# Kernel tuning notes

Measured on AMD Instinct MI355X. Metric: run time of the kernel, lower is better.

Reference implementation:

```python
import jax, jax.numpy as jnp
import numpy as np

N_NODES = 100000
N_EDGES = 1600000
D = 128


def setup_inputs() -> dict:
    key = jax.random.key(0)
    ks = jax.random.split(key, 8)
    s = lambda fan_in: 1.0 / np.sqrt(fan_in)
    return {
        "node_feature": jax.random.normal(ks[0], (N_NODES, D), dtype=jnp.float32),
        "src": jax.random.randint(ks[1], (N_EDGES,), 0, N_NODES),
        "dst": jax.random.randint(ks[2], (N_EDGES,), 0, N_NODES),
        "W1": jax.random.normal(ks[3], (2 * D, D), dtype=jnp.float32) * s(2 * D),
        "b1": jnp.zeros((D,), dtype=jnp.float32),
        "W2": jax.random.normal(ks[4], (D, D), dtype=jnp.float32) * s(D),
        "b2": jnp.zeros((D,), dtype=jnp.float32),
        "W3": jax.random.normal(ks[5], (D, D), dtype=jnp.float32) * s(D),
        "b3": jnp.zeros((D,), dtype=jnp.float32),
    }


def reference(node_feature, src, dst, W1, b1, W2, b2, W3, b3):
    n_nodes = node_feature.shape[0]
    # message: gather src node features over edges  [E, D]
    msg = node_feature[src]
    # reduce: sum messages into destination nodes   [N, D]
    agg = jax.ops.segment_sum(msg, dst, num_segments=n_nodes)
    # apply: concat(aggregated, own) -> MLP         [N, 2D] -> [N, D]
    inp = jnp.concatenate([agg, node_feature], axis=-1)
    h = jax.nn.relu(inp @ W1 + b1)
    h = jax.nn.relu(h @ W2 + b2)
    return h @ W3 + b3
```

## Files before the change

### kernel.cpp

```cpp
#include <hip/hip_runtime.h>

#define NNODES 100000
#define NEDGES 1600000
#define DD 128
#define BM 64
#define NBUCK 98
#define NBLK_MLP ((NNODES + BM - 1) / BM)
#define CAP 32
#define CAPB 20480
#define BIN1_WGS 391
#define BIN1_EPW 4096

#define WS_GCUR 100000
#define WS_BBASE 100128
#define WS_OFFS 100352
#define WS_ESRC 201216

#define WT1HI 0
#define WT1LO 32768
#define WT2HI 65536
#define WT2LO 81920
#define WT3HI 98304
#define WT3LO 114688

typedef __attribute__((ext_vector_type(8))) short short8;
typedef __attribute__((ext_vector_type(4))) float f32x4;

__device__ __forceinline__ void bf16_split(float x, ushort& hi, ushort& lo) {
  unsigned u = __float_as_uint(x);
  ushort h = (ushort)((u + 0x7FFFu + ((u >> 16) & 1u)) >> 16);
  float r = x - __uint_as_float(((unsigned)h) << 16);
  unsigned v = __float_as_uint(r);
  ushort l = (ushort)((v + 0x7FFFu + ((v >> 16) & 1u)) >> 16);
  hi = h;
  lo = l;
}

__device__ __forceinline__ void split8(const float4 v0, const float4 v1,
                                       short8& hi, short8& lo) {
  float x[8] = {v0.x, v0.y, v0.z, v0.w, v1.x, v1.y, v1.z, v1.w};
#pragma unroll
  for (int j = 0; j < 8; ++j) {
    ushort h, l;
    bf16_split(x[j], h, l);
    hi[j] = (short)h;
    lo[j] = (short)l;
  }
}

__global__ __launch_bounds__(256) void bin1_kernel(const int* __restrict__ src,
                                                   const int* __restrict__ dst,
                                                   int* __restrict__ gcur,
                                                   unsigned* __restrict__ ebuf) {
  __shared__ unsigned stage[NBUCK][CAP];
  __shared__ int scnt[NBUCK];
  const int t = threadIdx.x;
  for (int i = t; i < NBUCK; i += 256) scnt[i] = 0;
  __syncthreads();
  const int e0 = blockIdx.x * BIN1_EPW;
  for (int r = 0; r < BIN1_EPW / 1024; ++r) {
    unsigned item[4];
    int buck[4];
    int pend[4];
#pragma unroll
    for (int j = 0; j < 4; ++j) {
      pend[j] = 0;
      int e = e0 + r * 1024 + j * 256 + t;
      if (e < NEDGES) {
        int d = dst[e];
        int s = src[e];
        buck[j] = d >> 10;
        item[j] = ((unsigned)(d & 1023) << 17) | (unsigned)s;
        int p = atomicAdd(&scnt[buck[j]], 1);
        if (p < CAP)
          stage[buck[j]][p] = item[j];
        else
          pend[j] = 1;
      }
    }
    int pendLeft;
    do {
      __syncthreads();
      if (t < NBUCK && scnt[t] >= CAP) {
        int base = t * CAPB + atomicAdd(&gcur[t], CAP);
        for (int q = 0; q < CAP; ++q) ebuf[base + q] = stage[t][q];
        scnt[t] = 0;
      }
      __syncthreads();
      int mypend = 0;
#pragma unroll
      for (int j = 0; j < 4; ++j) {
        if (pend[j]) {
          int p = atomicAdd(&scnt[buck[j]], 1);
          if (p < CAP) {
            stage[buck[j]][p] = item[j];
            pend[j] = 0;
          } else {
            mypend = 1;
          }
        }
      }
      pendLeft = __syncthreads_count(mypend);
    } while (pendLeft > 0);
  }
  __syncthreads();
  if (t < NBUCK) {
    int n = scnt[t];
    if (n > 0) {
      int base = t * CAPB + atomicAdd(&gcur[t], n);
      for (int q = 0; q < n; ++q) ebuf[base + q] = stage[t][q];
    }
  }
}

__global__ __launch_bounds__(128) void bscan_kernel(const int* __restrict__ gcur,
                                                    int* __restrict__ bbase,
                                                    int* __restrict__ offs) {
  __shared__ int s[128];
  const int t = threadIdx.x;
  int v = (t < NBUCK) ? gcur[t] : 0;
  s[t] = v;
  __syncthreads();
  for (int off = 1; off < 128; off <<= 1) {
    int u = (t >= off) ? s[t - off] : 0;
    __syncthreads();
    s[t] += u;
    __syncthreads();
  }
  if (t < NBUCK) bbase[t] = s[t] - v;
  if (t == NBUCK - 1) offs[NNODES] = s[t];
}

__global__ __launch_bounds__(1024) void bucket_csr_kernel(const unsigned* __restrict__ ebuf,
                                                          const int* __restrict__ gcur,
                                                          const int* __restrict__ bbase,
                                                          int* __restrict__ offs,
                                                          int* __restrict__ esrc) {
  __shared__ int h[1024];
  __shared__ int cur[1024];
  const int t = threadIdx.x;
  const int c = blockIdx.x;
  const int n = gcur[c];
  const unsigned* eb = ebuf + c * CAPB;
  h[t] = 0;
  __syncthreads();
  for (int i = t; i < n; i += 1024) atomicAdd(&h[eb[i] >> 17], 1);
  __syncthreads();
  int v = h[t];
  for (int off = 1; off < 1024; off <<= 1) {
    int u = (t >= off) ? h[t - off] : 0;
    __syncthreads();
    h[t] += u;
    __syncthreads();
  }
  int excl = h[t] - v + bbase[c];
  int node = (c << 10) + t;
  if (node < NNODES) offs[node] = excl;
  cur[t] = excl;
  __syncthreads();
  for (int i = t; i < n; i += 1024) {
    unsigned e = eb[i];
    int p = atomicAdd(&cur[e >> 17], 1);
    esrc[p] = (int)(e & 0x1FFFFu);
  }
}

__global__ __launch_bounds__(256) void wprep_kernel(const float* __restrict__ W1,
                                                    const float* __restrict__ W2,
                                                    const float* __restrict__ W3,
                                                    ushort* __restrict__ wt) {
  int tid = blockIdx.x * 256 + threadIdx.x;
  const float* W;
  int dstHi, dstLo, k, col;
  if (tid < 32768) {
    int j = tid & 7, l = (tid >> 3) & 63, tile = tid >> 9;
    int kk = tile & 7, c16 = tile >> 3;
    k = kk * 32 + (l >> 4) * 8 + j;
    col = c16 * 16 + (l & 15);
    W = W1;
    dstHi = WT1HI + tid;
    dstLo = WT1LO + tid;
  } else {
    int t2 = tid - 32768;
    int which = t2 >> 14;
    int t1 = t2 & 16383;
    int j = t1 & 7, l = (t1 >> 3) & 63, tile = t1 >> 9;
    int kk = tile & 3, c16 = tile >> 2;
    k = kk * 32 + (l >> 4) * 8 + j;
    col = c16 * 16 + (l & 15);
    W = which ? W3 : W2;
    dstHi = (which ? WT3HI : WT2HI) + t1;
    dstLo = (which ? WT3LO : WT2LO) + t1;
  }
  ushort hi, lo;
  bf16_split(W[k * DD + col], hi, lo);
  wt[dstHi] = hi;
  wt[dstLo] = lo;
}


template <int KT>
__device__ __forceinline__ void lds_ksteps(const ushort* Hh, const ushort* Hl,
                                           const ushort* __restrict__ WhiT,
                                           const ushort* __restrict__ WloT,
                                           int tileOff, int wc2, int lane,
                                           int l15, int lhi, f32x4 acc[4][2]) {
#pragma unroll 2
  for (int kk = 0; kk < 4; ++kk) {
    short8 bhi[2], blo[2];
#pragma unroll
    for (int ct = 0; ct < 2; ++ct) {
      int tb = ((wc2 + ct) * KT + tileOff + kk) * 512 + lane * 8;
      bhi[ct] = *(const short8*)&WhiT[tb];
      blo[ct] = *(const short8*)&WloT[tb];
    }
#pragma unroll
    for (int rt = 0; rt < 4; ++rt) {
      int row = rt * 16 + l15;
      int byte = (row * 256 + kk * 64 + lhi * 16) ^ ((row & 7) << 4);
      short8 ahi = *(const short8*)((const char*)Hh + byte);
      short8 alo = *(const short8*)((const char*)Hl + byte);
#pragma unroll
      for (int ct = 0; ct < 2; ++ct) {
        acc[rt][ct] = __builtin_amdgcn_mfma_f32_16x16x32_bf16(ahi, bhi[ct], acc[rt][ct], 0, 0, 0);
        acc[rt][ct] = __builtin_amdgcn_mfma_f32_16x16x32_bf16(ahi, blo[ct], acc[rt][ct], 0, 0, 0);
        acc[rt][ct] = __builtin_amdgcn_mfma_f32_16x16x32_bf16(alo, bhi[ct], acc[rt][ct], 0, 0, 0);
      }
    }
  }
}

__device__ __forceinline__ void l1_step(const float* __restrict__ srcb,
                                        const ushort* __restrict__ wt,
                                        int kkTile, int kOff, const int rowA[4],
                                        int wc2, int lane, int lhi,
                                        f32x4 acc[4][2]) {
  short8 bhi[2], blo[2];
#pragma unroll
  for (int ct = 0; ct < 2; ++ct) {
    int tb = ((wc2 + ct) * 8 + kkTile) * 512 + lane * 8;
    bhi[ct] = *(const short8*)&wt[WT1HI + tb];
    blo[ct] = *(const short8*)&wt[WT1LO + tb];
  }
#pragma unroll
  for (int rt = 0; rt < 4; ++rt) {
    const float* p = srcb + rowA[rt] * DD + kOff + lhi * 8;
    float4 v0 = *(const float4*)p;
    float4 v1 = *(const float4*)(p + 4);
    short8 ahi, alo;
    split8(v0, v1, ahi, alo);
#pragma unroll
    for (int ct = 0; ct < 2; ++ct) {
      acc[rt][ct] = __builtin_amdgcn_mfma_f32_16x16x32_bf16(ahi, bhi[ct], acc[rt][ct], 0, 0, 0);
      acc[rt][ct] = __builtin_amdgcn_mfma_f32_16x16x32_bf16(ahi, blo[ct], acc[rt][ct], 0, 0, 0);
      acc[rt][ct] = __builtin_amdgcn_mfma_f32_16x16x32_bf16(alo, bhi[ct], acc[rt][ct], 0, 0, 0);
    }
  }
}

__device__ __forceinline__ void store_h(ushort* Hh, ushort* Hl,
                                        const float* __restrict__ b,
                                        int wc2, int l15, int lhi,
                                        f32x4 acc[4][2]) {
#pragma unroll
  for (int rt = 0; rt < 4; ++rt) {
#pragma unroll
    for (int ct = 0; ct < 2; ++ct) {
      int col = (wc2 + ct) * 16 + l15;
      float bias = b[col];
#pragma unroll
      for (int i = 0; i < 4; ++i) {
        int row = rt * 16 + lhi * 4 + i;
        float v = fmaxf(acc[rt][ct][i] + bias, 0.f);
        ushort h, l;
        bf16_split(v, h, l);
        int byte = (row * 256 + col * 2) ^ ((row & 7) << 4);
        *(ushort*)((char*)Hh + byte) = h;
        *(ushort*)((char*)Hl + byte) = l;
      }
    }
  }
}

__global__ __launch_bounds__(256, 5) void fused_kernel(const float* __restrict__ nf,
                                                       const int* __restrict__ offs,
                                                       const int* __restrict__ esrc,
                                                       const ushort* __restrict__ wt,
                                                       const float* __restrict__ b1,
                                                       const float* __restrict__ b2,
                                                       const float* __restrict__ b3,
                                                       float* __restrict__ out) {
  __shared__ ushort smem[16384];
  ushort* Xhi = smem;
  ushort* Xlo = smem + 8192;

  const int t = threadIdx.x;
  const int lane = t & 63;
  const int w = t >> 6;
  const int wc2 = w * 2;
  const int l15 = lane & 15;
  const int lhi = lane >> 4;
  const int base = blockIdx.x * BM;

  {
    const int g = t >> 5;
    const int l32 = t & 31;
    const int col = l32 << 2;
    for (int j = 0; j < 8; ++j) {
      const int r = g * 8 + j;
      const int node = base + r;
      if (node >= NNODES) break;
      float4 a0 = make_float4(0.f, 0.f, 0.f, 0.f);
      float4 a1 = make_float4(0.f, 0.f, 0.f, 0.f);
      float4 a2 = make_float4(0.f, 0.f, 0.f, 0.f);
      float4 a3 = make_float4(0.f, 0.f, 0.f, 0.f);
      const int beg = offs[node];
      const int end = offs[node + 1];
      int i = beg;
      int s0, s1, s2, s3;
      const bool have4 = (i + 3 < end);
      if (have4) {
        s0 = esrc[i]; s1 = esrc[i + 1]; s2 = esrc[i + 2]; s3 = esrc[i + 3];
      }
      for (; i + 7 < end; i += 4) {
        int n0 = esrc[i + 4], n1 = esrc[i + 5], n2 = esrc[i + 6], n3 = esrc[i + 7];
        float4 v0 = *(const float4*)&nf[s0 * DD + col];
        float4 v1 = *(const float4*)&nf[s1 * DD + col];
        float4 v2 = *(const float4*)&nf[s2 * DD + col];
        float4 v3 = *(const float4*)&nf[s3 * DD + col];
        a0.x += v0.x; a0.y += v0.y; a0.z += v0.z; a0.w += v0.w;
        a1.x += v1.x; a1.y += v1.y; a1.z += v1.z; a1.w += v1.w;
        a2.x += v2.x; a2.y += v2.y; a2.z += v2.z; a2.w += v2.w;
        a3.x += v3.x; a3.y += v3.y; a3.z += v3.z; a3.w += v3.w;
        s0 = n0; s1 = n1; s2 = n2; s3 = n3;
      }
      if (have4) {
        float4 v0 = *(const float4*)&nf[s0 * DD + col];
        float4 v1 = *(const float4*)&nf[s1 * DD + col];
        float4 v2 = *(const float4*)&nf[s2 * DD + col];
        float4 v3 = *(const float4*)&nf[s3 * DD + col];
        a0.x += v0.x; a0.y += v0.y; a0.z += v0.z; a0.w += v0.w;
        a1.x += v1.x; a1.y += v1.y; a1.z += v1.z; a1.w += v1.w;
        a2.x += v2.x; a2.y += v2.y; a2.z += v2.z; a2.w += v2.w;
        a3.x += v3.x; a3.y += v3.y; a3.z += v3.z; a3.w += v3.w;
        i += 4;
      }
      for (; i < end; ++i) {
        int s = esrc[i];
        float4 v0 = *(const float4*)&nf[s * DD + col];
        a0.x += v0.x; a0.y += v0.y; a0.z += v0.z; a0.w += v0.w;
      }
      a0.x += a1.x; a0.y += a1.y; a0.z += a1.z; a0.w += a1.w;
      a2.x += a3.x; a2.y += a3.y; a2.z += a3.z; a2.w += a3.w;
      a0.x += a2.x; a0.y += a2.y; a0.z += a2.z; a0.w += a2.w;
      ushort h0, h1, h2, h3, l0, l1, l2, l3;
      bf16_split(a0.x, h0, l0);
      bf16_split(a0.y, h1, l1);
      bf16_split(a0.z, h2, l2);
      bf16_split(a0.w, h3, l3);
      int byte = (r * 256 + col * 2) ^ ((r & 7) << 4);
      *(ushort4*)((char*)Xhi + byte) = make_ushort4(h0, h1, h2, h3);
      *(ushort4*)((char*)Xlo + byte) = make_ushort4(l0, l1, l2, l3);
    }
  }
  __syncthreads();

  int rowA[4];
#pragma unroll
  for (int rt = 0; rt < 4; ++rt) rowA[rt] = min(base + rt * 16 + l15, NNODES - 1);

  const f32x4 z = {0.f, 0.f, 0.f, 0.f};
  f32x4 acc[4][2];

#pragma unroll
  for (int rt = 0; rt < 4; ++rt)
#pragma unroll
    for (int ct = 0; ct < 2; ++ct) acc[rt][ct] = z;
  lds_ksteps<8>(Xhi, Xlo, wt + WT1HI, wt + WT1LO, 0, wc2, lane, l15, lhi, acc);
#pragma unroll 2
  for (int kk = 0; kk < 4; ++kk)
    l1_step(nf, wt, kk + 4, kk * 32, rowA, wc2, lane, lhi, acc);
  __syncthreads();
  store_h(Xhi, Xlo, b1, wc2, l15, lhi, acc);
  __syncthreads();

#pragma unroll
  for (int rt = 0; rt < 4; ++rt)
#pragma unroll
    for (int ct = 0; ct < 2; ++ct) acc[rt][ct] = z;
  lds_ksteps<4>(Xhi, Xlo, wt + WT2HI, wt + WT2LO, 0, wc2, lane, l15, lhi, acc);
  __syncthreads();
  store_h(Xhi, Xlo, b2, wc2, l15, lhi, acc);
  __syncthreads();

#pragma unroll
  for (int rt = 0; rt < 4; ++rt)
#pragma unroll
    for (int ct = 0; ct < 2; ++ct) acc[rt][ct] = z;
  lds_ksteps<4>(Xhi, Xlo, wt + WT3HI, wt + WT3LO, 0, wc2, lane, l15, lhi, acc);
#pragma unroll
  for (int rt = 0; rt < 4; ++rt) {
#pragma unroll
    for (int ct = 0; ct < 2; ++ct) {
      int col = (wc2 + ct) * 16 + l15;
      float bias = b3[col];
#pragma unroll
      for (int i = 0; i < 4; ++i) {
        int row = base + rt * 16 + lhi * 4 + i;
        if (row < NNODES) out[row * DD + col] = acc[rt][ct][i] + bias;
      }
    }
  }
}

extern "C" void kernel_launch(void* const* d_in, const int* in_sizes, int n_in,
                              void* d_out, int out_size, void* d_ws, size_t ws_size,
                              hipStream_t stream) {
  const float* nf = (const float*)d_in[0];
  const int* src = (const int*)d_in[1];
  const int* dst = (const int*)d_in[2];
  const float* W1 = (const float*)d_in[3];
  const float* b1 = (const float*)d_in[4];
  const float* W2 = (const float*)d_in[5];
  const float* b2 = (const float*)d_in[6];
  const float* W3 = (const float*)d_in[7];
  const float* b3 = (const float*)d_in[8];
  float* out = (float*)d_out;

  int* wsi = (int*)d_ws;
  int* gcur = wsi + WS_GCUR;
  int* bbase = wsi + WS_BBASE;
  int* offs = wsi + WS_OFFS;
  int* esrc = wsi + WS_ESRC;
  ushort* wt = (ushort*)wsi;

  unsigned* ebuf = (unsigned*)out;

  hipMemsetAsync(gcur, 0, NBUCK * sizeof(int), stream);
  bin1_kernel<<<BIN1_WGS, 256, 0, stream>>>(src, dst, gcur, ebuf);
  bscan_kernel<<<1, 128, 0, stream>>>(gcur, bbase, offs);
  bucket_csr_kernel<<<NBUCK, 1024, 0, stream>>>(ebuf, gcur, bbase, offs, esrc);
  wprep_kernel<<<256, 256, 0, stream>>>(W1, W2, W3, wt);
  fused_kernel<<<NBLK_MLP, 256, 0, stream>>>(nf, offs, esrc, wt, b1, b2, b3, out);
}
```

Baseline: 240.0 us.

## Double fused block to 512 threads with dynamic row assignment for aggregation

The fused gather+MLP kernel now runs 8 waves per block instead of 4. Each wave computes one 16-column strip instead of two, which halves per-thread accumulators. During aggregation, half-wave groups claim rows dynamically through an LDS atomic counter, so rows with many edges are load-balanced across groups. This costs an extra barrier and per-row atomics, and each wave now re-reads the same A fragments from LDS and global memory for fewer columns.

Measured after the change: 257.7 us. 7.4% more time.

```diff
diff --git a/kernel.cpp b/kernel.cpp
--- a/kernel.cpp
+++ b/kernel.cpp
@@ -199,90 +199,7 @@
 }
 
 
-template <int KT>
-__device__ __forceinline__ void lds_ksteps(const ushort* Hh, const ushort* Hl,
-                                           const ushort* __restrict__ WhiT,
-                                           const ushort* __restrict__ WloT,
-                                           int tileOff, int wc2, int lane,
-                                           int l15, int lhi, f32x4 acc[4][2]) {
-#pragma unroll 2
-  for (int kk = 0; kk < 4; ++kk) {
-    short8 bhi[2], blo[2];
-#pragma unroll
-    for (int ct = 0; ct < 2; ++ct) {
-      int tb = ((wc2 + ct) * KT + tileOff + kk) * 512 + lane * 8;
-      bhi[ct] = *(const short8*)&WhiT[tb];
-      blo[ct] = *(const short8*)&WloT[tb];
-    }
-#pragma unroll
-    for (int rt = 0; rt < 4; ++rt) {
-      int row = rt * 16 + l15;
-      int byte = (row * 256 + kk * 64 + lhi * 16) ^ ((row & 7) << 4);
-      short8 ahi = *(const short8*)((const char*)Hh + byte);
-      short8 alo = *(const short8*)((const char*)Hl + byte);
-#pragma unroll
-      for (int ct = 0; ct < 2; ++ct) {
-        acc[rt][ct] = __builtin_amdgcn_mfma_f32_16x16x32_bf16(ahi, bhi[ct], acc[rt][ct], 0, 0, 0);
-        acc[rt][ct] = __builtin_amdgcn_mfma_f32_16x16x32_bf16(ahi, blo[ct], acc[rt][ct], 0, 0, 0);
-        acc[rt][ct] = __builtin_amdgcn_mfma_f32_16x16x32_bf16(alo, bhi[ct], acc[rt][ct], 0, 0, 0);
-      }
-    }
-  }
-}
-
-__device__ __forceinline__ void l1_step(const float* __restrict__ srcb,
-                                        const ushort* __restrict__ wt,
-                                        int kkTile, int kOff, const int rowA[4],
-                                        int wc2, int lane, int lhi,
-                                        f32x4 acc[4][2]) {
-  short8 bhi[2], blo[2];
-#pragma unroll
-  for (int ct = 0; ct < 2; ++ct) {
-    int tb = ((wc2 + ct) * 8 + kkTile) * 512 + lane * 8;
-    bhi[ct] = *(const short8*)&wt[WT1HI + tb];
-    blo[ct] = *(const short8*)&wt[WT1LO + tb];
-  }
-#pragma unroll
-  for (int rt = 0; rt < 4; ++rt) {
-    const float* p = srcb + rowA[rt] * DD + kOff + lhi * 8;
-    float4 v0 = *(const float4*)p;
-    float4 v1 = *(const float4*)(p + 4);
-    short8 ahi, alo;
-    split8(v0, v1, ahi, alo);
-#pragma unroll
-    for (int ct = 0; ct < 2; ++ct) {
-      acc[rt][ct] = __builtin_amdgcn_mfma_f32_16x16x32_bf16(ahi, bhi[ct], acc[rt][ct], 0, 0, 0);
-      acc[rt][ct] = __builtin_amdgcn_mfma_f32_16x16x32_bf16(ahi, blo[ct], acc[rt][ct], 0, 0, 0);
-      acc[rt][ct] = __builtin_amdgcn_mfma_f32_16x16x32_bf16(alo, bhi[ct], acc[rt][ct], 0, 0, 0);
-    }
-  }
-}
-
-__device__ __forceinline__ void store_h(ushort* Hh, ushort* Hl,
-                                        const float* __restrict__ b,
-                                        int wc2, int l15, int lhi,
-                                        f32x4 acc[4][2]) {
-#pragma unroll
-  for (int rt = 0; rt < 4; ++rt) {
-#pragma unroll
-    for (int ct = 0; ct < 2; ++ct) {
-      int col = (wc2 + ct) * 16 + l15;
-      float bias = b[col];
-#pragma unroll
-      for (int i = 0; i < 4; ++i) {
-        int row = rt * 16 + lhi * 4 + i;
-        float v = fmaxf(acc[rt][ct][i] + bias, 0.f);
-        ushort h, l;
-        bf16_split(v, h, l);
-        int byte = (row * 256 + col * 2) ^ ((row & 7) << 4);
-        *(ushort*)((char*)Hh + byte) = h;
-        *(ushort*)((char*)Hl + byte) = l;
-      }
-    }
-  }
-}
-
-__global__ __launch_bounds__(256, 5) void fused_kernel(const float* __restrict__ nf,
+__global__ __launch_bounds__(512, 6) void fused_kernel(const float* __restrict__ nf,
                                                        const int* __restrict__ offs,
                                                        const int* __restrict__ esrc,
                                                        const ushort* __restrict__ wt,
@@ -291,23 +208,28 @@
                                                        const float* __restrict__ b3,
                                                        float* __restrict__ out) {
   __shared__ ushort smem[16384];
-  ushort* Xhi = smem;
-  ushort* Xlo = smem + 8192;
+  __shared__ int nextRow;
+  ushort* Xh = smem;
+  ushort* Xl = smem + 8192;
 
   const int t = threadIdx.x;
   const int lane = t & 63;
   const int w = t >> 6;
-  const int wc2 = w * 2;
   const int l15 = lane & 15;
   const int lhi = lane >> 4;
   const int base = blockIdx.x * BM;
 
+  if (t == 0) nextRow = 0;
+  __syncthreads();
+
   {
-    const int g = t >> 5;
     const int l32 = t & 31;
     const int col = l32 << 2;
-    for (int j = 0; j < 8; ++j) {
-      const int r = g * 8 + j;
+    for (;;) {
+      int r;
+      if (l32 == 0) r = atomicAdd(&nextRow, 1);
+      r = __shfl(r, 0, 32);
+      if (r >= BM) break;
       const int node = base + r;
       if (node >= NNODES) break;
       float4 a0 = make_float4(0.f, 0.f, 0.f, 0.f);
@@ -359,55 +281,134 @@
       bf16_split(a0.z, h2, l2);
       bf16_split(a0.w, h3, l3);
       int byte = (r * 256 + col * 2) ^ ((r & 7) << 4);
-      *(ushort4*)((char*)Xhi + byte) = make_ushort4(h0, h1, h2, h3);
-      *(ushort4*)((char*)Xlo + byte) = make_ushort4(l0, l1, l2, l3);
-    }
-  }
-  __syncthreads();
-
-  int rowA[4];
-#pragma unroll
-  for (int rt = 0; rt < 4; ++rt) rowA[rt] = min(base + rt * 16 + l15, NNODES - 1);
+      *(ushort4*)((char*)Xh + byte) = make_ushort4(h0, h1, h2, h3);
+      *(ushort4*)((char*)Xl + byte) = make_ushort4(l0, l1, l2, l3);
+    }
+  }
+  __syncthreads();
 
   const f32x4 z = {0.f, 0.f, 0.f, 0.f};
-  f32x4 acc[4][2];
-
-#pragma unroll
-  for (int rt = 0; rt < 4; ++rt)
-#pragma unroll
-    for (int ct = 0; ct < 2; ++ct) acc[rt][ct] = z;
-  lds_ksteps<8>(Xhi, Xlo, wt + WT1HI, wt + WT1LO, 0, wc2, lane, l15, lhi, acc);
+  const int mycol = w * 16 + l15;
+  f32x4 acc[4];
+
+#pragma unroll
+  for (int rt = 0; rt < 4; ++rt) acc[rt] = z;
+#pragma unroll
+  for (int kk = 0; kk < 4; ++kk) {
+    int tb = (w * 8 + kk) * 512 + lane * 8;
+    short8 bhi = *(const short8*)&wt[WT1HI + tb];
+    short8 blo = *(const short8*)&wt[WT1LO + tb];
+#pragma unroll
+    for (int rt = 0; rt < 4; ++rt) {
+      int row = rt * 16 + l15;
+      int byte = (row * 256 + kk * 64 + lhi * 16) ^ ((row & 7) << 4);
+      short8 ahi = *(const short8*)((const char*)Xh + byte);
+      short8 alo = *(const short8*)((const char*)Xl + byte);
+      acc[rt] = __builtin_amdgcn_mfma_f32_16x16x32_bf16(ahi, bhi, acc[rt], 0, 0, 0);
+      acc[rt] = __builtin_amdgcn_mfma_f32_16x16x32_bf16(ahi, blo, acc[rt], 0, 0, 0);
+      acc[rt] = __builtin_amdgcn_mfma_f32_16x16x32_bf16(alo, bhi, acc[rt], 0, 0, 0);
+    }
+  }
 #pragma unroll 2
-  for (int kk = 0; kk < 4; ++kk)
-    l1_step(nf, wt, kk + 4, kk * 32, rowA, wc2, lane, lhi, acc);
-  __syncthreads();
-  store_h(Xhi, Xlo, b1, wc2, l15, lhi, acc);
-  __syncthreads();
-
-#pragma unroll
-  for (int rt = 0; rt < 4; ++rt)
-#pragma unroll
-    for (int ct = 0; ct < 2; ++ct) acc[rt][ct] = z;
-  lds_ksteps<4>(Xhi, Xlo, wt + WT2HI, wt + WT2LO, 0, wc2, lane, l15, lhi, acc);
-  __syncthreads();
-  store_h(Xhi, Xlo, b2, wc2, l15, lhi, acc);
-  __syncthreads();
-
-#pragma unroll
-  for (int rt = 0; rt < 4; ++rt)
-#pragma unroll
-    for (int ct = 0; ct < 2; ++ct) acc[rt][ct] = z;
-  lds_ksteps<4>(Xhi, Xlo, wt + WT3HI, wt + WT3LO, 0, wc2, lane, l15, lhi, acc);
-#pragma unroll
-  for (int rt = 0; rt < 4; ++rt) {
-#pragma unroll
-    for (int ct = 0; ct < 2; ++ct) {
-      int col = (wc2 + ct) * 16 + l15;
-      float bias = b3[col];
+  for (int kk = 0; kk < 4; ++kk) {
+    int tb = (w * 8 + kk + 4) * 512 + lane * 8;
+    short8 bhi = *(const short8*)&wt[WT1HI + tb];
+    short8 blo = *(const short8*)&wt[WT1LO + tb];
+#pragma unroll
+    for (int rt = 0; rt < 4; ++rt) {
+      int rowg = min(base + rt * 16 + l15, NNODES - 1);
+      const float* p = nf + rowg * DD + kk * 32 + lhi * 8;
+      float4 v0 = *(const float4*)p;
+      float4 v1 = *(const float4*)(p + 4);
+      short8 ahi, alo;
+      split8(v0, v1, ahi, alo);
+      acc[rt] = __builtin_amdgcn_mfma_f32_16x16x32_bf16(ahi, bhi, acc[rt], 0, 0, 0);
+      acc[rt] = __builtin_amdgcn_mfma_f32_16x16x32_bf16(ahi, blo, acc[rt], 0, 0, 0);
+      acc[rt] = __builtin_amdgcn_mfma_f32_16x16x32_bf16(alo, bhi, acc[rt], 0, 0, 0);
+    }
+  }
+  __syncthreads();
+  {
+    float bias = b1[mycol];
+#pragma unroll
+    for (int rt = 0; rt < 4; ++rt) {
+#pragma unroll
+      for (int i = 0; i < 4; ++i) {
+        int row = rt * 16 + lhi * 4 + i;
+        float v = fmaxf(acc[rt][i] + bias, 0.f);
+        ushort h, l;
+        bf16_split(v, h, l);
+        int byte = (row * 256 + mycol * 2) ^ ((row & 7) << 4);
+        *(ushort*)((char*)Xh + byte) = h;
+        *(ushort*)((char*)Xl + byte) = l;
+      }
+    }
+  }
+  __syncthreads();
+
+#pragma unroll
+  for (int rt = 0; rt < 4; ++rt) acc[rt] = z;
+#pragma unroll
+  for (int kk = 0; kk < 4; ++kk) {
+    int tb = (w * 4 + kk) * 512 + lane * 8;
+    short8 bhi = *(const short8*)&wt[WT2HI + tb];
+    short8 blo = *(const short8*)&wt[WT2LO + tb];
+#pragma unroll
+    for (int rt = 0; rt < 4; ++rt) {
+      int row = rt * 16 + l15;
+      int byte = (row * 256 + kk * 64 + lhi * 16) ^ ((row & 7) << 4);
+      short8 ahi = *(const short8*)((const char*)Xh + byte);
+      short8 alo = *(const short8*)((const char*)Xl + byte);
+      acc[rt] = __builtin_amdgcn_mfma_f32_16x16x32_bf16(ahi, bhi, acc[rt], 0, 0, 0);
+      acc[rt] = __builtin_amdgcn_mfma_f32_16x16x32_bf16(ahi, blo, acc[rt], 0, 0, 0);
+      acc[rt] = __builtin_amdgcn_mfma_f32_16x16x32_bf16(alo, bhi, acc[rt], 0, 0, 0);
+    }
+  }
+  __syncthreads();
+  {
+    float bias = b2[mycol];
+#pragma unroll
+    for (int rt = 0; rt < 4; ++rt) {
+#pragma unroll
+      for (int i = 0; i < 4; ++i) {
+        int row = rt * 16 + lhi * 4 + i;
+        float v = fmaxf(acc[rt][i] + bias, 0.f);
+        ushort h, l;
+        bf16_split(v, h, l);
+        int byte = (row * 256 + mycol * 2) ^ ((row & 7) << 4);
+        *(ushort*)((char*)Xh + byte) = h;
+        *(ushort*)((char*)Xl + byte) = l;
+      }
+    }
+  }
+  __syncthreads();
+
+#pragma unroll
+  for (int rt = 0; rt < 4; ++rt) acc[rt] = z;
+#pragma unroll
+  for (int kk = 0; kk < 4; ++kk) {
+    int tb = (w * 4 + kk) * 512 + lane * 8;
+    short8 bhi = *(const short8*)&wt[WT3HI + tb];
+    short8 blo = *(const short8*)&wt[WT3LO + tb];
+#pragma unroll
+    for (int rt = 0; rt < 4; ++rt) {
+      int row = rt * 16 + l15;
+      int byte = (row * 256 + kk * 64 + lhi * 16) ^ ((row & 7) << 4);
+      short8 ahi = *(const short8*)((const char*)Xh + byte);
+      short8 alo = *(const short8*)((const char*)Xl + byte);
+      acc[rt] = __builtin_amdgcn_mfma_f32_16x16x32_bf16(ahi, bhi, acc[rt], 0, 0, 0);
+      acc[rt] = __builtin_amdgcn_mfma_f32_16x16x32_bf16(ahi, blo, acc[rt], 0, 0, 0);
+      acc[rt] = __builtin_amdgcn_mfma_f32_16x16x32_bf16(alo, bhi, acc[rt], 0, 0, 0);
+    }
+  }
+  {
+    float bias = b3[mycol];
+#pragma unroll
+    for (int rt = 0; rt < 4; ++rt) {
 #pragma unroll
       for (int i = 0; i < 4; ++i) {
         int row = base + rt * 16 + lhi * 4 + i;
-        if (row < NNODES) out[row * DD + col] = acc[rt][ct][i] + bias;
+        if (row < NNODES) out[row * DD + mycol] = acc[rt][i] + bias;
       }
     }
   }
@@ -441,5 +442,5 @@
   bscan_kernel<<<1, 128, 0, stream>>>(gcur, bbase, offs);
   bucket_csr_kernel<<<NBUCK, 1024, 0, stream>>>(ebuf, gcur, bbase, offs, esrc);
   wprep_kernel<<<256, 256, 0, stream>>>(W1, W2, W3, wt);
-  fused_kernel<<<NBLK_MLP, 256, 0, stream>>>(nf, offs, esrc, wt, b1, b2, b3, out);
-}
+  fused_kernel<<<NBLK_MLP, 512, 0, stream>>>(nf, offs, esrc, wt, b1, b2, b3, out);
+}
```
